# Optimization experiments

Hardware: AMD Instinct MI355X
Metric: run time of the kernel (lower is better)

The kernel has to match this reference:

```python
import jax, jax.numpy as jnp
import numpy as np

D_MODEL = 1024
N_HEADS = 16
D_K = D_MODEL // N_HEADS


def setup_inputs() -> dict:
    key = jax.random.key(0)
    ks = jax.random.split(key, 9)
    s = 0.02
    return {
        "x": jax.random.normal(ks[0], (4, 2048, D_MODEL), dtype=jnp.float32),
        "WQ_w": jax.random.normal(ks[1], (D_MODEL, D_MODEL), dtype=jnp.float32) * s,
        "WQ_b": jax.random.normal(ks[2], (D_MODEL,), dtype=jnp.float32) * s,
        "WK_w": jax.random.normal(ks[3], (D_MODEL, D_MODEL), dtype=jnp.float32) * s,
        "WK_b": jax.random.normal(ks[4], (D_MODEL,), dtype=jnp.float32) * s,
        "WV_w": jax.random.normal(ks[5], (D_MODEL, D_MODEL), dtype=jnp.float32) * s,
        "WV_b": jax.random.normal(ks[6], (D_MODEL,), dtype=jnp.float32) * s,
        "Wo_w": jax.random.normal(ks[7], (D_MODEL, D_MODEL), dtype=jnp.float32) * s,
        "Wo_b": jax.random.normal(ks[8], (D_MODEL,), dtype=jnp.float32) * s,
    }


def _rope_cache(T, dtype):
    half = D_K // 2
    freq = 1.0 / (10000.0 ** (2.0 * jnp.arange(half, dtype=dtype) / D_K))
    angles = jnp.arange(T, dtype=dtype)[:, None] * freq[None, :]  # [T, half]
    return jnp.cos(angles), jnp.sin(angles)


def _apply_rope(x, cos, sin):
    # x: [B, H, T, d_k]; cos/sin: [T, d_k//2] broadcast over B,H
    half = x.shape[-1] // 2
    x1, x2 = x[..., :half], x[..., half:]
    return jnp.concatenate([x1 * cos - x2 * sin, x1 * sin + x2 * cos], axis=-1)


def reference(x, WQ_w, WQ_b, WK_w, WK_b, WV_w, WV_b, Wo_w, Wo_b):
    B, T, D = x.shape

    def proj(w, b):
        y = jnp.einsum('btd,ed->bte', x, w) + b
        return y.reshape(B, T, N_HEADS, D_K).transpose(0, 2, 1, 3)  # [B,H,T,d_k]

    q = proj(WQ_w, WQ_b)
    k = proj(WK_w, WK_b)
    v = proj(WV_w, WV_b)

    cos, sin = _rope_cache(T, x.dtype)
    q = _apply_rope(q, cos, sin)
    k = _apply_rope(k, cos, sin)

    scores = jnp.einsum('bhqd,bhkd->bhqk', q, k) / jnp.sqrt(jnp.asarray(D_K, x.dtype))
    causal = jnp.tril(jnp.ones((T, T), dtype=bool))
    scores = jnp.where(causal[None, None, :, :], scores, -jnp.inf)
    attn = jax.nn.softmax(scores, axis=-1)
    out = jnp.einsum('bhqk,bhkd->bhqd', attn, v)
    out = out.transpose(0, 2, 1, 3).reshape(B, T, D)
    return jnp.einsum('btd,ed->bte', out, Wo_w) + Wo_b
```

## Files before the change

### kernel.cpp

```cpp
#include <hip/hip_runtime.h>
#include <math.h>

#define DM 1024
#define NH 16
#define DK 64
#define BB 4
#define TT 2048
#define MTOT (BB*TT)

typedef __bf16 bf16x8 __attribute__((ext_vector_type(8)));
typedef short  s16x4  __attribute__((ext_vector_type(4)));
typedef float  f32x4  __attribute__((ext_vector_type(4)));

__device__ __forceinline__ short f2bf_s(float f) {
    __bf16 h = (__bf16)f;
    return __builtin_bit_cast(short, h);
}

__device__ __forceinline__ float exp2_fast(float x) {
    float r;
    asm("v_exp_f32 %0, %1" : "=v"(r) : "v"(x));
    return r;
}

__device__ __forceinline__ void async_copy16(unsigned short* lds, const unsigned short* g) {
    __builtin_amdgcn_global_load_lds(
        (const __attribute__((address_space(1))) unsigned int*)g,
        (__attribute__((address_space(3))) unsigned int*)lds, 16, 0, 0);
}

__global__ __launch_bounds__(256)
void cvt_all_kernel(const float* __restrict__ x,
                    const float* __restrict__ wq, const float* __restrict__ wk,
                    const float* __restrict__ wv, const float* __restrict__ wo,
                    unsigned short* __restrict__ xb,
                    unsigned short* __restrict__ wqb, unsigned short* __restrict__ wkb,
                    unsigned short* __restrict__ wvb, unsigned short* __restrict__ wob)
{
    const int XB = (MTOT * DM) / 1024;
    int bz = blockIdx.x;
    const float* src; unsigned short* dst; int blk;
    if (bz < XB) { src = x; dst = xb; blk = bz; }
    else {
        int t = bz - XB, which = t >> 10;
        blk = t & 1023;
        if (which == 0)      { src = wq; dst = wqb; }
        else if (which == 1) { src = wk; dst = wkb; }
        else if (which == 2) { src = wv; dst = wvb; }
        else                 { src = wo; dst = wob; }
    }
    int i = blk * 256 + threadIdx.x;
    float4 v = ((const float4*)src)[i];
    ushort4 o;
    o.x = (unsigned short)f2bf_s(v.x); o.y = (unsigned short)f2bf_s(v.y);
    o.z = (unsigned short)f2bf_s(v.z); o.w = (unsigned short)f2bf_s(v.w);
    ((ushort4*)dst)[i] = o;
}

template<int MODE>
__global__ __launch_bounds__(256, 3)
void gemm_bf16_kernel(const unsigned short* __restrict__ X,
                      const unsigned short* __restrict__ W0, const float* __restrict__ b0,
                      const unsigned short* __restrict__ W1, const float* __restrict__ b1,
                      const unsigned short* __restrict__ W2, const float* __restrict__ b2,
                      void* __restrict__ Y0, void* __restrict__ Y1, void* __restrict__ Y2)
{
    const unsigned short* W; const float* bias; void* Yv;
    const int z = blockIdx.z;
    if (z == 0)      { W = W0; bias = b0; Yv = Y0; }
    else if (z == 1) { W = W1; bias = b1; Yv = Y1; }
    else             { W = W2; bias = b2; Yv = Y2; }

    __shared__ __align__(16) unsigned short As[128 * 64];
    __shared__ __align__(16) unsigned short Bs[128 * 64];

    const int tid  = threadIdx.x;
    const int w    = tid >> 6, lane = tid & 63;
    const int quad = lane >> 4, lq = lane & 15;
    const int bm = blockIdx.x * 128, bn = blockIdx.y * 128;
    const int wm = (w >> 1) * 64,   wn = (w & 1) * 64;

    const int srow = lane >> 3;
    const int sg   = (lane & 7) ^ srow;
    const int soff = sg * 8;

    f32x4 acc[4][4];
    #pragma unroll
    for (int i = 0; i < 4; ++i)
        #pragma unroll
        for (int j = 0; j < 4; ++j)
            acc[i][j] = {0.f, 0.f, 0.f, 0.f};

    for (int k0 = 0; k0 < DM; k0 += 64) {
        #pragma unroll
        for (int c = 0; c < 4; ++c) {
            int r0 = w * 32 + c * 8;
            async_copy16(&As[r0 * 64], &X[(size_t)(bm + r0 + srow) * DM + k0 + soff]);
            async_copy16(&Bs[r0 * 64], &W[(size_t)(bn + r0 + srow) * DM + k0 + soff]);
        }
        __syncthreads();

        #pragma unroll
        for (int ks = 0; ks < 2; ++ks) {
            const int gsw = ((ks << 2) + quad) ^ (lq & 7);
            bf16x8 af[4], bfr[4];
            #pragma unroll
            for (int i = 0; i < 4; ++i)
                af[i] = *(const bf16x8*)&As[(wm + i*16 + lq) * 64 + gsw * 8];
            #pragma unroll
            for (int j = 0; j < 4; ++j)
                bfr[j] = *(const bf16x8*)&Bs[(wn + j*16 + lq) * 64 + gsw * 8];
            #pragma unroll
            for (int i = 0; i < 4; ++i)
                #pragma unroll
                for (int j = 0; j < 4; ++j)
                    acc[i][j] = __builtin_amdgcn_mfma_f32_16x16x32_bf16(af[i], bfr[j], acc[i][j], 0, 0, 0);
        }
        __syncthreads();
    }

    if (MODE == 0) {
        #pragma unroll
        for (int j = 0; j < 4; ++j) {
            int n = bn + wn + j*16 + lq;
            float bv = bias[n];
            #pragma unroll
            for (int i = 0; i < 4; ++i)
                #pragma unroll
                for (int r = 0; r < 4; ++r) {
                    int m = bm + wm + i*16 + quad*4 + r;
                    ((float*)Yv)[(size_t)m * DM + n] = acc[i][j][r] + bv;
                }
        }
    } else if (z == 2) {
        #pragma unroll
        for (int j = 0; j < 4; ++j) {
            int n = bn + wn + j*16 + lq;
            float bv = bias[n];
            int h = n >> 6, dk = n & 63;
            #pragma unroll
            for (int i = 0; i < 4; ++i)
                #pragma unroll
                for (int r = 0; r < 4; ++r) {
                    int m = bm + wm + i*16 + quad*4 + r;
                    int b = m >> 11, t = m & 2047;
                    ((__bf16*)Yv)[(((size_t)(b * NH + h) * TT + t) << 6) + dk] =
                        (__bf16)(acc[i][j][r] + bv);
                }
        }
    } else {
        const float QSC = (z == 0) ? 0.125f * 1.44269504f : 1.0f;
        const int h = (bn + wn) >> 6;
        #pragma unroll
        for (int jp = 0; jp < 2; ++jp) {
            int dk1 = jp * 16 + lq;
            float freq = exp2f(-(float)dk1 * 0.4152410118f);
            float bv1 = bias[bn + wn + dk1];
            float bv2 = bias[bn + wn + dk1 + 32];
            #pragma unroll
            for (int i = 0; i < 4; ++i) {
                #pragma unroll
                for (int r = 0; r < 4; ++r) {
                    int m = bm + wm + i*16 + quad*4 + r;
                    int b = m >> 11, t = m & 2047;
                    float ang = (float)t * freq;
                    float sn = __sinf(ang), cs = __cosf(ang);
                    float v1 = acc[i][jp][r]     + bv1;
                    float v2 = acc[i][jp + 2][r] + bv2;
                    float o1 = (v1 * cs - v2 * sn) * QSC;
                    float o2 = (v1 * sn + v2 * cs) * QSC;
                    size_t base = ((size_t)(b * NH + h) * TT + t) << 6;
                    ((__bf16*)Yv)[base + dk1]      = (__bf16)o1;
                    ((__bf16*)Yv)[base + dk1 + 32] = (__bf16)o2;
                }
            }
        }
    }
}

__global__ __launch_bounds__(256)
void vtrans_kernel(const unsigned short* __restrict__ V, unsigned short* __restrict__ Vt)
{
    __shared__ unsigned short tile[64][72];
    const int tid = threadIdx.x;
    const int t0 = blockIdx.x * 64;
    const int bh = blockIdx.y;
    const size_t ib = (size_t)bh * TT * DK;
    const size_t ob = (size_t)bh * DK * TT;
    #pragma unroll
    for (int p = 0; p < 2; ++p) {
        int s = p * 256 + tid;
        int r = s >> 3, c0 = (s & 7) * 8;
        *(uint4*)&tile[r][c0] = *(const uint4*)&V[ib + (size_t)(t0 + r) * DK + c0];
    }
    __syncthreads();
    #pragma unroll
    for (int p = 0; p < 2; ++p) {
        int s = p * 256 + tid;
        int dk = s >> 3, c0 = (s & 7) * 8;
        unsigned short tmp[8];
        #pragma unroll
        for (int e = 0; e < 8; ++e) tmp[e] = tile[c0 + e][dk];
        *(uint4*)&Vt[ob + (size_t)dk * TT + t0 + c0] = *(const uint4*)tmp;
    }
}

__global__ __launch_bounds__(256, 3)
void attn_kernel(const unsigned short* __restrict__ Q, const unsigned short* __restrict__ K,
                 const unsigned short* __restrict__ Vt_g, unsigned short* __restrict__ ctx)
{
    __shared__ __align__(16) unsigned short KV[2][2][64 * 64];

    const int tid  = threadIdx.x;
    const int w    = tid >> 6, lane = tid & 63;
    const int quad = lane >> 4, lq = lane & 15;
    const int bh = blockIdx.x;
    const int x  = blockIdx.y;
    const int qt[2] = { x, 31 - x };
    const size_t kbase = (size_t)bh * TT * DK;
    const size_t vbase = (size_t)bh * DK * TT;

    const int srow = lane >> 3;
    const int sg   = (lane & 7) ^ srow;
    const unsigned short* Ksrc = &K[kbase + (size_t)(w*16 + srow) * DK + sg*8];
    const unsigned short* Vsrc = &Vt_g[vbase + (size_t)(w*16 + srow) * TT + sg*8];

    auto issue = [&](int kb, int buf) {
        unsigned short* Kd = &KV[buf][0][w*16*64];
        unsigned short* Vd = &KV[buf][1][w*16*64];
        const unsigned short* ks0 = Ksrc + (size_t)kb * 64 * DK;
        const unsigned short* vs0 = Vsrc + (size_t)kb * 64;
        async_copy16(Kd,          ks0);
        async_copy16(Kd + 8*64,   ks0 + 8*DK);
        async_copy16(Vd,          vs0);
        async_copy16(Vd + 8*64,   vs0 + (size_t)8*TT);
    };

    int   qrow[2];
    bf16x8 qf[2][2];
    #pragma unroll
    for (int i = 0; i < 2; ++i) {
        qrow[i] = qt[i]*64 + w*16 + lq;
        qf[i][0] = *(const bf16x8*)&Q[kbase + (size_t)qrow[i] * DK + quad*8];
        qf[i][1] = *(const bf16x8*)&Q[kbase + (size_t)qrow[i] * DK + 32 + quad*8];
    }

    f32x4 accO[2][4];
    float l_i[2] = {0.f, 0.f};
    #pragma unroll
    for (int i = 0; i < 2; ++i)
        #pragma unroll
        for (int dt = 0; dt < 4; ++dt) accO[i][dt] = {0.f,0.f,0.f,0.f};

    const int kbmax = qt[1];
    issue(0, 0);
    for (int kb = 0; kb <= kbmax; ++kb) {
        __syncthreads();
        if (kb < kbmax) issue(kb + 1, (kb + 1) & 1);

        const unsigned short* Kb_ = &KV[kb & 1][0][0];
        const unsigned short* Vb_ = &KV[kb & 1][1][0];

        bf16x8 kf[2][4];
        #pragma unroll
        for (int ks = 0; ks < 2; ++ks)
            #pragma unroll
            for (int nt = 0; nt < 4; ++nt)
                kf[ks][nt] = *(const bf16x8*)&Kb_[(nt*16 + lq) * 64 +
                                (((ks << 2) + quad) ^ (lq & 7)) * 8];

        s16x4 p[2][4];
        #pragma unroll
        for (int i = 0; i < 2; ++i) {
            if (kb <= qt[i]) {
                f32x4 st[4];
                #pragma unroll
                for (int nt = 0; nt < 4; ++nt) st[nt] = {0.f,0.f,0.f,0.f};
                __builtin_amdgcn_s_setprio(1);
                #pragma unroll
                for (int ks = 0; ks < 2; ++ks)
                    #pragma unroll
                    for (int nt = 0; nt < 4; ++nt)
                        st[nt] = __builtin_amdgcn_mfma_f32_16x16x32_bf16(kf[ks][nt], qf[i][ks], st[nt], 0, 0, 0);
                __builtin_amdgcn_s_setprio(0);
                if (kb == qt[i]) {
                    #pragma unroll
                    for (int nt = 0; nt < 4; ++nt)
                        #pragma unroll
                        for (int r = 0; r < 4; ++r) {
                            int kc = kb*64 + nt*16 + quad*4 + r;
                            if (kc > qrow[i]) st[nt][r] = -1e30f;
                        }
                }
                #pragma unroll
                for (int nt = 0; nt < 4; ++nt)
                    #pragma unroll
                    for (int r = 0; r < 4; ++r) {
                        float e = exp2_fast(st[nt][r]);
                        l_i[i] += e;
                        p[i][nt][r] = f2bf_s(e);
                    }
            }
        }

        #pragma unroll
        for (int ktp = 0; ktp < 2; ++ktp) {
            s16x4 vbh[2][4];
            #pragma unroll
            for (int k2 = 0; k2 < 2; ++k2) {
                int kt = ktp*2 + k2;
                #pragma unroll
                for (int dt = 0; dt < 4; ++dt)
                    vbh[k2][dt] = *(const s16x4*)&Vb_[(dt*16 + lq) * 64 +
                                    (((kt << 1) + (quad >> 1)) ^ (lq & 7)) * 8 +
                                    (quad & 1) * 4];
            }
            __builtin_amdgcn_s_setprio(1);
            #pragma unroll
            for (int i = 0; i < 2; ++i) {
                if (kb <= qt[i]) {
                    #pragma unroll
                    for (int k2 = 0; k2 < 2; ++k2)
                        #pragma unroll
                        for (int dt = 0; dt < 4; ++dt)
                            accO[i][dt] = __builtin_amdgcn_mfma_f32_16x16x16bf16_1k(
                                p[i][ktp*2 + k2], vbh[k2][dt], accO[i][dt], 0, 0, 0);
                }
            }
            __builtin_amdgcn_s_setprio(0);
        }
    }

    const int b = bh >> 4, h = bh & 15;
    #pragma unroll
    for (int i = 0; i < 2; ++i) {
        float l = l_i[i];
        l += __shfl_xor(l, 16, 64);
        l += __shfl_xor(l, 32, 64);
        float linv = 1.0f / l;
        f32x4 il4;
        #pragma unroll
        for (int r = 0; r < 4; ++r) il4[r] = __shfl(linv, quad*4 + r, 64);
        #pragma unroll
        for (int r = 0; r < 4; ++r) {
            int t = qt[i]*64 + w*16 + quad*4 + r;
            size_t ob = ((size_t)b * TT + t) * DM + h * DK;
            #pragma unroll
            for (int dt = 0; dt < 4; ++dt)
                ((__bf16*)ctx)[ob + dt*16 + lq] = (__bf16)(accO[i][dt][r] * il4[r]);
        }
    }
}

extern "C" void kernel_launch(void* const* d_in, const int* in_sizes, int n_in,
                              void* d_out, int out_size, void* d_ws, size_t ws_size,
                              hipStream_t stream)
{
    const float* x   = (const float*)d_in[0];
    const float* WQw = (const float*)d_in[1];
    const float* WQb = (const float*)d_in[2];
    const float* WKw = (const float*)d_in[3];
    const float* WKb = (const float*)d_in[4];
    const float* WVw = (const float*)d_in[5];
    const float* WVb = (const float*)d_in[6];
    const float* WOw = (const float*)d_in[7];
    const float* WOb = (const float*)d_in[8];
    float* out = (float*)d_out;

    unsigned short* ws  = (unsigned short*)d_ws;
    unsigned short* xb  = ws;
    unsigned short* wqb = xb  + (size_t)MTOT * DM;
    unsigned short* wkb = wqb + (size_t)DM * DM;
    unsigned short* wvb = wkb + (size_t)DM * DM;
    unsigned short* wob = wvb + (size_t)DM * DM;
    unsigned short* Qb  = wob + (size_t)DM * DM;
    unsigned short* Kb  = Qb  + (size_t)MTOT * DM;
    unsigned short* Vb  = Kb  + (size_t)MTOT * DM;
    unsigned short* Vtb = Vb  + (size_t)MTOT * DM;
    unsigned short* ctxb = Vb;

    cvt_all_kernel<<<(MTOT*DM)/1024 + 4*(DM*DM)/1024, 256, 0, stream>>>(
        x, WQw, WKw, WVw, WOw, xb, wqb, wkb, wvb, wob);

    gemm_bf16_kernel<1><<<dim3(MTOT/128, DM/128, 3), 256, 0, stream>>>(
        xb, wqb, WQb, wkb, WKb, wvb, WVb, Qb, Kb, Vb);

    vtrans_kernel<<<dim3(TT/64, BB*NH), 256, 0, stream>>>(Vb, Vtb);

    attn_kernel<<<dim3(BB*NH, 16), 256, 0, stream>>>(Qb, Kb, Vtb, ctxb);

    gemm_bf16_kernel<0><<<dim3(MTOT/128, DM/128, 1), 256, 0, stream>>>(
        ctxb, wob, WOb, wob, WOb, wob, WOb, out, out, out);
}
```

Before: 247.4 us.

## Fuse V transpose into QKV GEMM epilogue and remap attention query-tile pairing

The V projection epilogue now writes V directly in transposed [b,h,dk,t] layout using 4-element packed bf16 stores. This lets the separate vtrans kernel and its extra round trip through global memory be dropped. The attention grid also changes its query-tile pairing from (x, 31-x) to (t, t+16), dispatched through a fixed permutation table. That pairing gives uneven causal work per block, and the transposed epilogue stores are strided 8-byte writes, which may cost some GEMM store efficiency.

```diff
diff --git a/kernel.cpp b/kernel.cpp
--- a/kernel.cpp
+++ b/kernel.cpp
@@ -139,14 +139,16 @@
             float bv = bias[n];
             int h = n >> 6, dk = n & 63;
             #pragma unroll
-            for (int i = 0; i < 4; ++i)
-                #pragma unroll
-                for (int r = 0; r < 4; ++r) {
-                    int m = bm + wm + i*16 + quad*4 + r;
-                    int b = m >> 11, t = m & 2047;
-                    ((__bf16*)Yv)[(((size_t)(b * NH + h) * TT + t) << 6) + dk] =
-                        (__bf16)(acc[i][j][r] + bv);
-                }
+            for (int i = 0; i < 4; ++i) {
+                int m0 = bm + wm + i*16 + quad*4;
+                int b = m0 >> 11, t0 = m0 & 2047;
+                ushort4 o;
+                o.x = (unsigned short)f2bf_s(acc[i][j][0] + bv);
+                o.y = (unsigned short)f2bf_s(acc[i][j][1] + bv);
+                o.z = (unsigned short)f2bf_s(acc[i][j][2] + bv);
+                o.w = (unsigned short)f2bf_s(acc[i][j][3] + bv);
+                *(ushort4*)&((unsigned short*)Yv)[((size_t)(b * NH + h) * DK + dk) * TT + t0] = o;
+            }
         }
     } else {
         const float QSC = (z == 0) ? 0.125f * 1.44269504f : 1.0f;
@@ -178,33 +180,6 @@
     }
 }
 
-__global__ __launch_bounds__(256)
-void vtrans_kernel(const unsigned short* __restrict__ V, unsigned short* __restrict__ Vt)
-{
-    __shared__ unsigned short tile[64][72];
-    const int tid = threadIdx.x;
-    const int t0 = blockIdx.x * 64;
-    const int bh = blockIdx.y;
-    const size_t ib = (size_t)bh * TT * DK;
-    const size_t ob = (size_t)bh * DK * TT;
-    #pragma unroll
-    for (int p = 0; p < 2; ++p) {
-        int s = p * 256 + tid;
-        int r = s >> 3, c0 = (s & 7) * 8;
-        *(uint4*)&tile[r][c0] = *(const uint4*)&V[ib + (size_t)(t0 + r) * DK + c0];
-    }
-    __syncthreads();
-    #pragma unroll
-    for (int p = 0; p < 2; ++p) {
-        int s = p * 256 + tid;
-        int dk = s >> 3, c0 = (s & 7) * 8;
-        unsigned short tmp[8];
-        #pragma unroll
-        for (int e = 0; e < 8; ++e) tmp[e] = tile[c0 + e][dk];
-        *(uint4*)&Vt[ob + (size_t)dk * TT + t0 + c0] = *(const uint4*)tmp;
-    }
-}
-
 __global__ __launch_bounds__(256, 3)
 void attn_kernel(const unsigned short* __restrict__ Q, const unsigned short* __restrict__ K,
                  const unsigned short* __restrict__ Vt_g, unsigned short* __restrict__ ctx)
@@ -215,8 +190,10 @@
     const int w    = tid >> 6, lane = tid & 63;
     const int quad = lane >> 4, lq = lane & 15;
     const int bh = blockIdx.x;
-    const int x  = blockIdx.y;
-    const int qt[2] = { x, 31 - x };
+    const int s  = blockIdx.y;
+    const int tmap[16] = {15,12,13,14, 8,11,10,9, 7,4,5,6, 0,3,2,1};
+    const int t_lo = tmap[s];
+    const int qt[2] = { t_lo, t_lo + 16 };
     const size_t kbase = (size_t)bh * TT * DK;
     const size_t vbase = (size_t)bh * DK * TT;
 
@@ -383,9 +360,7 @@
         x, WQw, WKw, WVw, WOw, xb, wqb, wkb, wvb, wob);
 
     gemm_bf16_kernel<1><<<dim3(MTOT/128, DM/128, 3), 256, 0, stream>>>(
-        xb, wqb, WQb, wkb, WKb, wvb, WVb, Qb, Kb, Vb);
-
-    vtrans_kernel<<<dim3(TT/64, BB*NH), 256, 0, stream>>>(Vb, Vtb);
+        xb, wqb, WQb, wkb, WKb, wvb, WVb, Qb, Kb, Vtb);
 
     attn_kernel<<<dim3(BB*NH, 16), 256, 0, stream>>>(Qb, Kb, Vtb, ctxb);
 
```

Measured after the change: 241.2 us. -2.5%, faster.
